# Kernel tuning notes

Measured on AMD Instinct MI355X. Metric: run time of the kernel, lower is better.

## Reference

```python
import jax, jax.numpy as jnp
import numpy as np
import math

H = 16          # num heads
D = 64          # size_per_head
HID = H * D     # 1024
ROT = 32        # rotary_hsize <= D//2


def setup_inputs() -> dict:
    key = jax.random.key(0)
    ks = jax.random.split(key, 10)
    B, S = 2, 2048
    x = jax.random.normal(ks[0], (B, S, HID), dtype=jnp.float32)
    sinusoids = jax.random.normal(ks[1], (B, 2, S, ROT), dtype=jnp.float32)
    attention_bias = jnp.zeros((B, 1, S, S), dtype=jnp.float32)
    scale = 1.0 / math.sqrt(HID)
    Wq = jax.random.normal(ks[2], (HID, HID), dtype=jnp.float32) * scale
    bq = jnp.zeros((HID,), dtype=jnp.float32)
    Wk = jax.random.normal(ks[3], (HID, HID), dtype=jnp.float32) * scale
    bk = jnp.zeros((HID,), dtype=jnp.float32)
    Wv = jax.random.normal(ks[4], (HID, HID), dtype=jnp.float32) * scale
    bv = jnp.zeros((HID,), dtype=jnp.float32)
    Wo = jax.random.normal(ks[5], (HID, HID), dtype=jnp.float32) * scale
    return {"x": x, "sinusoids": sinusoids, "attention_bias": attention_bias,
            "Wq": Wq, "bq": bq, "Wk": Wk, "bk": bk, "Wv": Wv, "bv": bv, "Wo": Wo}


def _apply_rotary(qk, sin, cos):
    # qk: [B,S,H,D]; sin/cos: [B,S,1,ROT]
    r = qk[..., :ROT]
    # stack([-even, odd], -1).reshape -> interleaved (-x0, x1, -x2, x3, ...)
    rt = jnp.stack([-r[..., ::2], r[..., 1::2]], axis=-1).reshape(r.shape)
    return jnp.concatenate([r * cos + rt * sin, qk[..., ROT:]], axis=-1)


def reference(x, sinusoids, attention_bias, Wq, bq, Wk, bk, Wv, bv, Wo):
    B, S, _ = x.shape
    q = (x @ Wq + bq).reshape(B, S, H, D)
    k = (x @ Wk + bk).reshape(B, S, H, D)
    v = (x @ Wv + bv).reshape(B, S, H, D)
    sin = sinusoids[..., 0, :, None, :]  # [B,S,1,ROT]
    cos = sinusoids[..., 1, :, None, :]
    q = _apply_rotary(q, sin, cos)
    k = _apply_rotary(k, sin, cos)
    q = q / math.sqrt(D)
    scores = jnp.einsum('bqhd,bkhd->bhqk', q, k) + attention_bias
    probs = jax.nn.softmax(scores, axis=-1)
    out = jnp.einsum('bhqk,bkhd->bqhd', probs, v).reshape(B, S, HID)
    return out @ Wo
```

## Files before the change

kernel.cpp:

```cpp
#include <hip/hip_runtime.h>
#include <hip/hip_bf16.h>

#define H_   16
#define D_   64
#define HID  1024
#define S_   2048
#define B_   2
#define M_   (B_*S_)
#define ROT  32
#define LOG2E 1.44269504088896341f
#define QSCALE (0.125f * LOG2E)

typedef __bf16 bf16x8 __attribute__((ext_vector_type(8)));
typedef float  f32x4  __attribute__((ext_vector_type(4)));

#define XB_OFF   0u
#define WQT_OFF  (8u<<20)
#define WKT_OFF  (10u<<20)
#define WVT_OFF  (12u<<20)
#define WOT_OFF  (14u<<20)
#define F_OFF    (16u<<20)
#define QH_OFF   ((16u<<20) + (1u<<19))
#define KH_OFF   (QH_OFF + (8u<<20))
#define VT_OFF   (KH_OFF + (8u<<20))
#define AB_OFF   (VT_OFF + (8u<<20))

__device__ __forceinline__ float fexp2(float x) {
#if __has_builtin(__builtin_amdgcn_exp2f)
  return __builtin_amdgcn_exp2f(x);
#else
  return __expf(x * 0.69314718055994531f);
#endif
}

__device__ __forceinline__ unsigned pk2(float a, float b) {
  union { unsigned u; __bf16 h[2]; } w;
  w.h[0] = (__bf16)a; w.h[1] = (__bf16)b;
  return w.u;
}

__global__ __launch_bounds__(256) void convx_kernel(const float* __restrict__ x,
                                                    __hip_bfloat16* __restrict__ xb,
                                                    int* __restrict__ flag) {
  if (blockIdx.x == 0 && threadIdx.x == 0) *flag = 0;
  int i = (blockIdx.x * 256 + threadIdx.x) * 4;
  float4 v = *(const float4*)(x + i);
  union { __hip_bfloat16 h[4]; uint2 u; } o;
  o.h[0] = __float2bfloat16(v.x);
  o.h[1] = __float2bfloat16(v.y);
  o.h[2] = __float2bfloat16(v.z);
  o.h[3] = __float2bfloat16(v.w);
  *(uint2*)(xb + i) = o.u;
}

__global__ __launch_bounds__(256) void biaschk_kernel(const float* __restrict__ ab,
                                                      int* __restrict__ flag) {
  size_t i = ((size_t)blockIdx.x * 256 + threadIdx.x) * 16;
  const uint4* p = (const uint4*)(ab + i);
  unsigned acc = 0;
  #pragma unroll
  for (int j = 0; j < 4; j++) {
    uint4 u = p[j];
    acc |= u.x | u.y | u.z | u.w;
  }
  if (acc) *flag = 1;
}

__global__ __launch_bounds__(256) void rotf_kernel(const float* __restrict__ sinu,
                                                   float* __restrict__ F) {
  int i = blockIdx.x * 256 + threadIdx.x;
  int d  = i & (ROT-1);
  int bs = i >> 5;
  int s  = bs & (S_-1);
  int b  = bs >> 11;
  float sn = sinu[(((size_t)b*2 + 0)*S_ + s)*ROT + d];
  float cs = sinu[(((size_t)b*2 + 1)*S_ + s)*ROT + d];
  F[i] = cs + ((d & 1) ? sn : -sn);
}

__global__ __launch_bounds__(256) void wtrans_kernel(const float* __restrict__ W0, const float* __restrict__ W1,
                                                     const float* __restrict__ W2, const float* __restrict__ W3,
                                                     __hip_bfloat16* __restrict__ T0, __hip_bfloat16* __restrict__ T1,
                                                     __hip_bfloat16* __restrict__ T2, __hip_bfloat16* __restrict__ T3) {
  __shared__ float tile[32][33];
  const float* W = (blockIdx.z==0) ? W0 : (blockIdx.z==1) ? W1 : (blockIdx.z==2) ? W2 : W3;
  __hip_bfloat16* T = (blockIdx.z==0) ? T0 : (blockIdx.z==1) ? T1 : (blockIdx.z==2) ? T2 : T3;
  int bx = blockIdx.x * 32;
  int by = blockIdx.y * 32;
  int tx = threadIdx.x, ty = threadIdx.y;
  #pragma unroll
  for (int i = 0; i < 4; i++)
    tile[ty + i*8][tx] = W[(size_t)(by + ty + i*8)*HID + bx + tx];
  __syncthreads();
  #pragma unroll
  for (int i = 0; i < 4; i++)
    T[(size_t)(bx + ty + i*8)*HID + by + tx] = __float2bfloat16(tile[tx][ty + i*8]);
}

__global__ __launch_bounds__(256) void qkv_kernel(const __hip_bfloat16* __restrict__ A,
                                                  const __hip_bfloat16* __restrict__ Bt,
                                                  const float* __restrict__ bq,
                                                  const float* __restrict__ bk,
                                                  const float* __restrict__ bv,
                                                  const float* __restrict__ F,
                                                  __hip_bfloat16* __restrict__ Qh,
                                                  __hip_bfloat16* __restrict__ Kh,
                                                  __hip_bfloat16* __restrict__ Vt) {
  __shared__ __align__(16) __bf16 Asm[2][128*32];
  __shared__ __align__(16) __bf16 Bsm[2][64*32];
  int tid  = threadIdx.x;
  int lane = tid & 63;
  int wv   = tid >> 6;
  int lr   = lane & 15;
  int qd   = lane >> 4;
  int row0 = blockIdx.y * 128;
  int col0 = blockIdx.x * 64;
  int proj = col0 >> 10;
  int nb   = col0 & 1023;
  const float* bias = (proj == 0) ? bq : ((proj == 1) ? bk : bv);

  int cg = ((tid & 3) ^ ((tid >> 2) & 3)) * 8;
  const __bf16* Ag = (const __bf16*)A  + (size_t)(row0 + (tid >> 2)) * HID + cg;
  const __bf16* Bg = (const __bf16*)Bt + (size_t)(col0 + (tid >> 2)) * HID + cg;

  f32x4 acc[2][4] = {};

  auto stage = [&](int buf, int k0) {
    __builtin_amdgcn_global_load_lds(Ag + k0,                  &Asm[buf][wv*512],        16, 0, 0);
    __builtin_amdgcn_global_load_lds(Ag + (size_t)64*HID + k0, &Asm[buf][2048 + wv*512], 16, 0, 0);
    __builtin_amdgcn_global_load_lds(Bg + k0,                  &Bsm[buf][wv*512],        16, 0, 0);
  };

  stage(0, 0);
  int buf = 0;
  for (int k0 = 0; k0 < HID; k0 += 32, buf ^= 1) {
    __syncthreads();
    if (k0 + 32 < HID) stage(buf ^ 1, k0 + 32);
    const __bf16* As = &Asm[buf][0];
    const __bf16* Bs = &Bsm[buf][0];
    bf16x8 a[2], b[4];
    #pragma unroll
    for (int i = 0; i < 2; i++) {
      int row = wv*32 + i*16 + lr;
      a[i] = *(const bf16x8*)(As + row*32 + ((qd ^ (row & 3)) * 8));
    }
    #pragma unroll
    for (int t = 0; t < 4; t++) {
      int row = t*16 + lr;
      b[t] = *(const bf16x8*)(Bs + row*32 + ((qd ^ (row & 3)) * 8));
    }
    #pragma unroll
    for (int i = 0; i < 2; i++)
      #pragma unroll
      for (int t = 0; t < 4; t++)
        acc[i][t] = __builtin_amdgcn_mfma_f32_16x16x32_bf16(a[i], b[t], acc[i][t], 0, 0, 0);
  }

  #pragma unroll
  for (int i = 0; i < 2; i++) {
    #pragma unroll
    for (int t = 0; t < 4; t++) {
      int nl = nb + t*16 + lr;
      int h  = nl >> 6, d = nl & 63;
      if (proj == 2) {
        int m0 = row0 + wv*32 + i*16 + qd*4;
        int b2 = m0 >> 11, s0 = m0 & (S_-1);
        union { uint2 u; __bf16 hh[4]; } w;
        #pragma unroll
        for (int r = 0; r < 4; r++)
          w.hh[r] = (__bf16)(acc[i][t][r] + bias[nl]);
        *(uint2*)((__bf16*)Vt + ((size_t)(b2*H_ + h)*D_ + d)*S_ + s0) = w.u;
      } else {
        __hip_bfloat16* dst = (proj == 0) ? Qh : Kh;
        #pragma unroll
        for (int r = 0; r < 4; r++) {
          int m = row0 + wv*32 + i*16 + qd*4 + r;
          int b2 = m >> 11, s = m & (S_-1);
          float v = acc[i][t][r] + bias[nl];
          if (d < ROT) v *= F[(size_t)(b2*S_ + s)*ROT + d];
          if (proj == 0) v *= QSCALE;
          dst[((size_t)(b2*H_ + h)*S_ + s)*D_ + d] = __float2bfloat16(v);
        }
      }
    }
  }
}

__global__ __launch_bounds__(256) void gemm_o(const __hip_bfloat16* __restrict__ A,
                                              const __hip_bfloat16* __restrict__ Bt,
                                              float* __restrict__ out) {
  __shared__ __align__(16) __bf16 Asm[2][128*32];
  __shared__ __align__(16) __bf16 Bsm[2][64*32];
  int tid  = threadIdx.x;
  int lane = tid & 63;
  int wv   = tid >> 6;
  int lr   = lane & 15;
  int qd   = lane >> 4;
  int row0 = blockIdx.y * 128;
  int col0 = blockIdx.x * 64;
  int cg = ((tid & 3) ^ ((tid >> 2) & 3)) * 8;
  const __bf16* Ag = (const __bf16*)A  + (size_t)(row0 + (tid >> 2)) * HID + cg;
  const __bf16* Bg = (const __bf16*)Bt + (size_t)(col0 + (tid >> 2)) * HID + cg;

  f32x4 acc[2][4] = {};
  auto stage = [&](int buf, int k0) {
    __builtin_amdgcn_global_load_lds(Ag + k0,                  &Asm[buf][wv*512],        16, 0, 0);
    __builtin_amdgcn_global_load_lds(Ag + (size_t)64*HID + k0, &Asm[buf][2048 + wv*512], 16, 0, 0);
    __builtin_amdgcn_global_load_lds(Bg + k0,                  &Bsm[buf][wv*512],        16, 0, 0);
  };
  stage(0, 0);
  int buf = 0;
  for (int k0 = 0; k0 < HID; k0 += 32, buf ^= 1) {
    __syncthreads();
    if (k0 + 32 < HID) stage(buf ^ 1, k0 + 32);
    const __bf16* As = &Asm[buf][0];
    const __bf16* Bs = &Bsm[buf][0];
    bf16x8 a[2], b[4];
    #pragma unroll
    for (int i = 0; i < 2; i++) {
      int row = wv*32 + i*16 + lr;
      a[i] = *(const bf16x8*)(As + row*32 + ((qd ^ (row & 3)) * 8));
    }
    #pragma unroll
    for (int t = 0; t < 4; t++) {
      int row = t*16 + lr;
      b[t] = *(const bf16x8*)(Bs + row*32 + ((qd ^ (row & 3)) * 8));
    }
    #pragma unroll
    for (int i = 0; i < 2; i++)
      #pragma unroll
      for (int t = 0; t < 4; t++)
        acc[i][t] = __builtin_amdgcn_mfma_f32_16x16x32_bf16(a[i], b[t], acc[i][t], 0, 0, 0);
  }
  #pragma unroll
  for (int i = 0; i < 2; i++)
    #pragma unroll
    for (int t = 0; t < 4; t++)
      #pragma unroll
      for (int r = 0; r < 4; r++) {
        int m = row0 + wv*32 + i*16 + qd*4 + r;
        int n = col0 + t*16 + lr;
        out[(size_t)m*HID + n] = acc[i][t][r];
      }
}

#define PSTRIDE 72
__global__ __launch_bounds__(256) void flash_kernel(const __hip_bfloat16* __restrict__ Qh,
                                                    const __hip_bfloat16* __restrict__ Kh,
                                                    const __hip_bfloat16* __restrict__ Vt,
                                                    const float* __restrict__ abias,
                                                    const int* __restrict__ flag,
                                                    __hip_bfloat16* __restrict__ Ab) {
  __shared__ __align__(16) __bf16 Ksm[2][64*64];
  __shared__ __align__(16) __bf16 Vsm[2][64*64];
  __shared__ __align__(16) __bf16 Pb[4][32*PSTRIDE];
  int tid  = threadIdx.x;
  int lane = tid & 63;
  int wv   = tid >> 6;
  int lr   = lane & 15;
  int qd   = lane >> 4;
  int bh = blockIdx.y;
  int b  = bh >> 4;
  int h  = bh & 15;
  int q0 = blockIdx.x * 128 + wv * 32;

  const __bf16* Kbase = (const __bf16*)Kh + (size_t)bh*S_*D_;
  const __bf16* Vbase = (const __bf16*)Vt + (size_t)bh*D_*S_;

  const __bf16* Qp = (const __bf16*)Qh + ((size_t)bh*S_ + q0 + lr)*D_ + qd*8;
  bf16x8 qa00 = *(const bf16x8*)(Qp);
  bf16x8 qa01 = *(const bf16x8*)(Qp + 32);
  bf16x8 qa10 = *(const bf16x8*)(Qp + 16*D_);
  bf16x8 qa11 = *(const bf16x8*)(Qp + 16*D_ + 32);

  int hasbias = *flag;
  const float* bp0 = abias + (size_t)b*S_*S_ + (size_t)(q0 + lr)*S_;
  const float* bp1 = bp0 + (size_t)16*S_;

  int rowb = tid >> 3;
  int cg8  = ((tid & 7) ^ (rowb & 7)) * 8;

  auto stageKV = [&](int bf, int kt2) {
    __builtin_amdgcn_global_load_lds(Kbase + (size_t)(kt2 + rowb)*D_ + cg8,      &Ksm[bf][wv*512],        16, 0, 0);
    __builtin_amdgcn_global_load_lds(Kbase + (size_t)(kt2 + 32 + rowb)*D_ + cg8, &Ksm[bf][2048 + wv*512], 16, 0, 0);
    __builtin_amdgcn_global_load_lds(Vbase + (size_t)rowb*S_ + kt2 + cg8,        &Vsm[bf][wv*512],        16, 0, 0);
    __builtin_amdgcn_global_load_lds(Vbase + (size_t)(32 + rowb)*S_ + kt2 + cg8, &Vsm[bf][2048 + wv*512], 16, 0, 0);
  };

  f32x4 oacc0[4] = {}, oacc1[4] = {};
  float lsum0 = 0.f, lsum1 = 0.f;
  __bf16* P = &Pb[wv][0];
  int sw = lr & 7;

  stageKV(0, 0);
  int buf = 0;
  for (int kt = 0; kt < S_; kt += 64, buf ^= 1) {
    __syncthreads();
    if (kt + 64 < S_) stageKV(buf ^ 1, kt + 64);

    bf16x8 kf0[4], kf1[4];
    #pragma unroll
    for (int c = 0; c < 4; c++) {
      const __bf16* Kr = &Ksm[buf][(c*16 + lr)*64];
      kf0[c] = *(const bf16x8*)(Kr + ((qd       ^ sw) * 8));
      kf1[c] = *(const bf16x8*)(Kr + (((4 + qd) ^ sw) * 8));
    }
    f32x4 s0[4], s1[4];
    #pragma unroll
    for (int c = 0; c < 4; c++) {
      f32x4 z = {};
      z     = __builtin_amdgcn_mfma_f32_16x16x32_bf16(kf0[c], qa00, z, 0, 0, 0);
      s0[c] = __builtin_amdgcn_mfma_f32_16x16x32_bf16(kf1[c], qa01, z, 0, 0, 0);
      f32x4 z2 = {};
      z2    = __builtin_amdgcn_mfma_f32_16x16x32_bf16(kf0[c], qa10, z2, 0, 0, 0);
      s1[c] = __builtin_amdgcn_mfma_f32_16x16x32_bf16(kf1[c], qa11, z2, 0, 0, 0);
    }
    bf16x8 vf0[4], vf1[4];
    #pragma unroll
    for (int t = 0; t < 4; t++) {
      const __bf16* Vr = &Vsm[buf][(t*16 + lr)*64];
      vf0[t] = *(const bf16x8*)(Vr + ((qd       ^ sw) * 8));
      vf1[t] = *(const bf16x8*)(Vr + (((4 + qd) ^ sw) * 8));
    }
    if (hasbias) {
      #pragma unroll
      for (int c = 0; c < 4; c++) {
        float4 b0 = *(const float4*)(bp0 + kt + c*16 + qd*4);
        float4 b1 = *(const float4*)(bp1 + kt + c*16 + qd*4);
        s0[c][0] += b0.x*LOG2E; s0[c][1] += b0.y*LOG2E; s0[c][2] += b0.z*LOG2E; s0[c][3] += b0.w*LOG2E;
        s1[c][0] += b1.x*LOG2E; s1[c][1] += b1.y*LOG2E; s1[c][2] += b1.z*LOG2E; s1[c][3] += b1.w*LOG2E;
      }
    }
    #pragma unroll
    for (int c = 0; c < 4; c++) {
      float p0 = fexp2(s0[c][0]), p1 = fexp2(s0[c][1]), p2 = fexp2(s0[c][2]), p3 = fexp2(s0[c][3]);
      lsum0 += (p0 + p1) + (p2 + p3);
      *(unsigned*)(P + lr*PSTRIDE + c*16 + qd*4)     = pk2(p0, p1);
      *(unsigned*)(P + lr*PSTRIDE + c*16 + qd*4 + 2) = pk2(p2, p3);
      float r0 = fexp2(s1[c][0]), r1 = fexp2(s1[c][1]), r2 = fexp2(s1[c][2]), r3 = fexp2(s1[c][3]);
      lsum1 += (r0 + r1) + (r2 + r3);
      *(unsigned*)(P + (16+lr)*PSTRIDE + c*16 + qd*4)     = pk2(r0, r1);
      *(unsigned*)(P + (16+lr)*PSTRIDE + c*16 + qd*4 + 2) = pk2(r2, r3);
    }
    asm volatile("s_waitcnt lgkmcnt(0)" ::: "memory");
    bf16x8 pb00 = *(const bf16x8*)(P + lr*PSTRIDE + qd*8);
    bf16x8 pb01 = *(const bf16x8*)(P + lr*PSTRIDE + 32 + qd*8);
    bf16x8 pb10 = *(const bf16x8*)(P + (16+lr)*PSTRIDE + qd*8);
    bf16x8 pb11 = *(const bf16x8*)(P + (16+lr)*PSTRIDE + 32 + qd*8);
    #pragma unroll
    for (int t = 0; t < 4; t++) {
      oacc0[t] = __builtin_amdgcn_mfma_f32_16x16x32_bf16(vf0[t], pb00, oacc0[t], 0, 0, 0);
      oacc0[t] = __builtin_amdgcn_mfma_f32_16x16x32_bf16(vf1[t], pb01, oacc0[t], 0, 0, 0);
      oacc1[t] = __builtin_amdgcn_mfma_f32_16x16x32_bf16(vf0[t], pb10, oacc1[t], 0, 0, 0);
      oacc1[t] = __builtin_amdgcn_mfma_f32_16x16x32_bf16(vf1[t], pb11, oacc1[t], 0, 0, 0);
    }
  }

  lsum0 += __shfl_xor(lsum0, 16); lsum0 += __shfl_xor(lsum0, 32);
  lsum1 += __shfl_xor(lsum1, 16); lsum1 += __shfl_xor(lsum1, 32);
  float inv0 = 1.0f / lsum0;
  float inv1 = 1.0f / lsum1;
  size_t ro0 = ((size_t)(b*S_ + q0 + lr))*HID + h*D_;
  size_t ro1 = ((size_t)(b*S_ + q0 + 16 + lr))*HID + h*D_;
  #pragma unroll
  for (int t = 0; t < 4; t++) {
    union { uint2 u; __bf16 hh[4]; } w0, w1;
    #pragma unroll
    for (int r = 0; r < 4; r++) {
      w0.hh[r] = (__bf16)(oacc0[t][r]*inv0);
      w1.hh[r] = (__bf16)(oacc1[t][r]*inv1);
    }
    *(uint2*)((__bf16*)Ab + ro0 + t*16 + qd*4) = w0.u;
    *(uint2*)((__bf16*)Ab + ro1 + t*16 + qd*4) = w1.u;
  }
}

extern "C" void kernel_launch(void* const* d_in, const int* in_sizes, int n_in,
                              void* d_out, int out_size, void* d_ws, size_t ws_size,
                              hipStream_t stream) {
  (void)in_sizes; (void)n_in; (void)out_size; (void)ws_size;
  const float* x     = (const float*)d_in[0];
  const float* sinu  = (const float*)d_in[1];
  const float* abias = (const float*)d_in[2];
  const float* Wq    = (const float*)d_in[3];
  const float* bq    = (const float*)d_in[4];
  const float* Wk    = (const float*)d_in[5];
  const float* bk    = (const float*)d_in[6];
  const float* Wv    = (const float*)d_in[7];
  const float* bv    = (const float*)d_in[8];
  const float* Wo    = (const float*)d_in[9];

  char* ws = (char*)d_ws;
  __hip_bfloat16* Xb  = (__hip_bfloat16*)(ws + XB_OFF);
  __hip_bfloat16* Wqt = (__hip_bfloat16*)(ws + WQT_OFF);
  __hip_bfloat16* Wkt = (__hip_bfloat16*)(ws + WKT_OFF);
  __hip_bfloat16* Wvt = (__hip_bfloat16*)(ws + WVT_OFF);
  __hip_bfloat16* Wot = (__hip_bfloat16*)(ws + WOT_OFF);
  float*          F   = (float*)(ws + F_OFF);
  __hip_bfloat16* Qh  = (__hip_bfloat16*)(ws + QH_OFF);
  __hip_bfloat16* Kh  = (__hip_bfloat16*)(ws + KH_OFF);
  __hip_bfloat16* Vt  = (__hip_bfloat16*)(ws + VT_OFF);
  __hip_bfloat16* Ab  = (__hip_bfloat16*)(ws + AB_OFF);
  int* flag = (int*)d_out;

  convx_kernel<<<(M_*HID)/(256*4), 256, 0, stream>>>(x, Xb, flag);
  rotf_kernel<<<(B_*S_*ROT)/256, 256, 0, stream>>>(sinu, F);
  wtrans_kernel<<<dim3(HID/32, HID/32, 4), dim3(32, 8), 0, stream>>>(
      Wq, Wk, Wv, Wo, Wqt, Wkt, Wvt, Wot);
  biaschk_kernel<<<(B_*S_*S_)/(256*16), 256, 0, stream>>>(abias, flag);

  qkv_kernel<<<dim3(3*HID/64, M_/128), 256, 0, stream>>>(
      Xb, Wqt, bq, bk, bv, F, Qh, Kh, Vt);

  flash_kernel<<<dim3(S_/128, B_*H_), 256, 0, stream>>>(Qh, Kh, Vt, abias, flag, Ab);

  gemm_o<<<dim3(HID/64, M_/128), 256, 0, stream>>>(Ab, Wot, (float*)d_out);
}
```

Baseline: 249.0 us.

## Enlarge GEMM tiles to 128x128 and remap flash blocks for XCD locality

The QKV and output-projection GEMMs are merged into one templated kernel that uses a 128x128 block tile, with each wave computing a 64x64 sub-tile (4x4 MFMA accumulators) instead of 32x64. The aim is more operand reuse per LDS load, at the cost of higher register pressure and fewer blocks. Flash attention is changed to a 1D grid remapped so that all query blocks of the same batch-head land on the same XCD, which should improve L2 reuse of K/V.

```diff
diff --git a/kernel.cpp b/kernel.cpp
--- a/kernel.cpp
+++ b/kernel.cpp
@@ -97,38 +97,40 @@
     T[(size_t)(bx + ty + i*8)*HID + by + tx] = __float2bfloat16(tile[tx][ty + i*8]);
 }
 
-__global__ __launch_bounds__(256) void qkv_kernel(const __hip_bfloat16* __restrict__ A,
-                                                  const __hip_bfloat16* __restrict__ Bt,
-                                                  const float* __restrict__ bq,
-                                                  const float* __restrict__ bk,
-                                                  const float* __restrict__ bv,
-                                                  const float* __restrict__ F,
-                                                  __hip_bfloat16* __restrict__ Qh,
-                                                  __hip_bfloat16* __restrict__ Kh,
-                                                  __hip_bfloat16* __restrict__ Vt) {
+template<int MODE>
+__global__ __launch_bounds__(256) void gemm128(const __hip_bfloat16* __restrict__ A,
+                                               const __hip_bfloat16* __restrict__ Bt,
+                                               const float* __restrict__ bq,
+                                               const float* __restrict__ bk,
+                                               const float* __restrict__ bv,
+                                               const float* __restrict__ F,
+                                               __hip_bfloat16* __restrict__ Qh,
+                                               __hip_bfloat16* __restrict__ Kh,
+                                               __hip_bfloat16* __restrict__ Vt,
+                                               float* __restrict__ outf) {
   __shared__ __align__(16) __bf16 Asm[2][128*32];
-  __shared__ __align__(16) __bf16 Bsm[2][64*32];
+  __shared__ __align__(16) __bf16 Bsm[2][128*32];
   int tid  = threadIdx.x;
   int lane = tid & 63;
   int wv   = tid >> 6;
   int lr   = lane & 15;
   int qd   = lane >> 4;
   int row0 = blockIdx.y * 128;
-  int col0 = blockIdx.x * 64;
-  int proj = col0 >> 10;
-  int nb   = col0 & 1023;
-  const float* bias = (proj == 0) ? bq : ((proj == 1) ? bk : bv);
+  int col0 = blockIdx.x * 128;
+  int wrow = (wv >> 1) * 64;
+  int wcol = (wv & 1) * 64;
 
   int cg = ((tid & 3) ^ ((tid >> 2) & 3)) * 8;
   const __bf16* Ag = (const __bf16*)A  + (size_t)(row0 + (tid >> 2)) * HID + cg;
   const __bf16* Bg = (const __bf16*)Bt + (size_t)(col0 + (tid >> 2)) * HID + cg;
 
-  f32x4 acc[2][4] = {};
+  f32x4 acc[4][4] = {};
 
   auto stage = [&](int buf, int k0) {
     __builtin_amdgcn_global_load_lds(Ag + k0,                  &Asm[buf][wv*512],        16, 0, 0);
     __builtin_amdgcn_global_load_lds(Ag + (size_t)64*HID + k0, &Asm[buf][2048 + wv*512], 16, 0, 0);
     __builtin_amdgcn_global_load_lds(Bg + k0,                  &Bsm[buf][wv*512],        16, 0, 0);
+    __builtin_amdgcn_global_load_lds(Bg + (size_t)64*HID + k0, &Bsm[buf][2048 + wv*512], 16, 0, 0);
   };
 
   stage(0, 0);
@@ -138,32 +140,49 @@
     if (k0 + 32 < HID) stage(buf ^ 1, k0 + 32);
     const __bf16* As = &Asm[buf][0];
     const __bf16* Bs = &Bsm[buf][0];
-    bf16x8 a[2], b[4];
-    #pragma unroll
-    for (int i = 0; i < 2; i++) {
-      int row = wv*32 + i*16 + lr;
+    bf16x8 a[4], b[4];
+    #pragma unroll
+    for (int i = 0; i < 4; i++) {
+      int row = wrow + i*16 + lr;
       a[i] = *(const bf16x8*)(As + row*32 + ((qd ^ (row & 3)) * 8));
     }
     #pragma unroll
     for (int t = 0; t < 4; t++) {
-      int row = t*16 + lr;
+      int row = wcol + t*16 + lr;
       b[t] = *(const bf16x8*)(Bs + row*32 + ((qd ^ (row & 3)) * 8));
     }
     #pragma unroll
-    for (int i = 0; i < 2; i++)
+    for (int i = 0; i < 4; i++)
       #pragma unroll
       for (int t = 0; t < 4; t++)
         acc[i][t] = __builtin_amdgcn_mfma_f32_16x16x32_bf16(a[i], b[t], acc[i][t], 0, 0, 0);
   }
 
-  #pragma unroll
-  for (int i = 0; i < 2; i++) {
+  if (MODE == 1) {
+    #pragma unroll
+    for (int i = 0; i < 4; i++)
+      #pragma unroll
+      for (int t = 0; t < 4; t++)
+        #pragma unroll
+        for (int r = 0; r < 4; r++) {
+          int m = row0 + wrow + i*16 + qd*4 + r;
+          int n = col0 + wcol + t*16 + lr;
+          outf[(size_t)m*HID + n] = acc[i][t][r];
+        }
+    return;
+  }
+
+  int proj = col0 >> 10;
+  int nb   = (col0 & 1023) + wcol;
+  const float* bias = (proj == 0) ? bq : ((proj == 1) ? bk : bv);
+  #pragma unroll
+  for (int i = 0; i < 4; i++) {
     #pragma unroll
     for (int t = 0; t < 4; t++) {
       int nl = nb + t*16 + lr;
       int h  = nl >> 6, d = nl & 63;
       if (proj == 2) {
-        int m0 = row0 + wv*32 + i*16 + qd*4;
+        int m0 = row0 + wrow + i*16 + qd*4;
         int b2 = m0 >> 11, s0 = m0 & (S_-1);
         union { uint2 u; __bf16 hh[4]; } w;
         #pragma unroll
@@ -174,7 +193,7 @@
         __hip_bfloat16* dst = (proj == 0) ? Qh : Kh;
         #pragma unroll
         for (int r = 0; r < 4; r++) {
-          int m = row0 + wv*32 + i*16 + qd*4 + r;
+          int m = row0 + wrow + i*16 + qd*4 + r;
           int b2 = m >> 11, s = m & (S_-1);
           float v = acc[i][t][r] + bias[nl];
           if (d < ROT) v *= F[(size_t)(b2*S_ + s)*ROT + d];
@@ -184,64 +203,6 @@
       }
     }
   }
-}
-
-__global__ __launch_bounds__(256) void gemm_o(const __hip_bfloat16* __restrict__ A,
-                                              const __hip_bfloat16* __restrict__ Bt,
-                                              float* __restrict__ out) {
-  __shared__ __align__(16) __bf16 Asm[2][128*32];
-  __shared__ __align__(16) __bf16 Bsm[2][64*32];
-  int tid  = threadIdx.x;
-  int lane = tid & 63;
-  int wv   = tid >> 6;
-  int lr   = lane & 15;
-  int qd   = lane >> 4;
-  int row0 = blockIdx.y * 128;
-  int col0 = blockIdx.x * 64;
-  int cg = ((tid & 3) ^ ((tid >> 2) & 3)) * 8;
-  const __bf16* Ag = (const __bf16*)A  + (size_t)(row0 + (tid >> 2)) * HID + cg;
-  const __bf16* Bg = (const __bf16*)Bt + (size_t)(col0 + (tid >> 2)) * HID + cg;
-
-  f32x4 acc[2][4] = {};
-  auto stage = [&](int buf, int k0) {
-    __builtin_amdgcn_global_load_lds(Ag + k0,                  &Asm[buf][wv*512],        16, 0, 0);
-    __builtin_amdgcn_global_load_lds(Ag + (size_t)64*HID + k0, &Asm[buf][2048 + wv*512], 16, 0, 0);
-    __builtin_amdgcn_global_load_lds(Bg + k0,                  &Bsm[buf][wv*512],        16, 0, 0);
-  };
-  stage(0, 0);
-  int buf = 0;
-  for (int k0 = 0; k0 < HID; k0 += 32, buf ^= 1) {
-    __syncthreads();
-    if (k0 + 32 < HID) stage(buf ^ 1, k0 + 32);
-    const __bf16* As = &Asm[buf][0];
-    const __bf16* Bs = &Bsm[buf][0];
-    bf16x8 a[2], b[4];
-    #pragma unroll
-    for (int i = 0; i < 2; i++) {
-      int row = wv*32 + i*16 + lr;
-      a[i] = *(const bf16x8*)(As + row*32 + ((qd ^ (row & 3)) * 8));
-    }
-    #pragma unroll
-    for (int t = 0; t < 4; t++) {
-      int row = t*16 + lr;
-      b[t] = *(const bf16x8*)(Bs + row*32 + ((qd ^ (row & 3)) * 8));
-    }
-    #pragma unroll
-    for (int i = 0; i < 2; i++)
-      #pragma unroll
-      for (int t = 0; t < 4; t++)
-        acc[i][t] = __builtin_amdgcn_mfma_f32_16x16x32_bf16(a[i], b[t], acc[i][t], 0, 0, 0);
-  }
-  #pragma unroll
-  for (int i = 0; i < 2; i++)
-    #pragma unroll
-    for (int t = 0; t < 4; t++)
-      #pragma unroll
-      for (int r = 0; r < 4; r++) {
-        int m = row0 + wv*32 + i*16 + qd*4 + r;
-        int n = col0 + t*16 + lr;
-        out[(size_t)m*HID + n] = acc[i][t][r];
-      }
 }
 
 #define PSTRIDE 72
@@ -259,10 +220,14 @@
   int wv   = tid >> 6;
   int lr   = lane & 15;
   int qd   = lane >> 4;
-  int bh = blockIdx.y;
+  int idx  = blockIdx.x;
+  int xcd  = idx & 7;
+  int slot = idx >> 3;
+  int bh   = xcd * 4 + (slot >> 4);
+  int qblk = slot & 15;
   int b  = bh >> 4;
   int h  = bh & 15;
-  int q0 = blockIdx.x * 128 + wv * 32;
+  int q0 = qblk * 128 + wv * 32;
 
   const __bf16* Kbase = (const __bf16*)Kh + (size_t)bh*S_*D_;
   const __bf16* Vbase = (const __bf16*)Vt + (size_t)bh*D_*S_;
@@ -409,10 +374,11 @@
       Wq, Wk, Wv, Wo, Wqt, Wkt, Wvt, Wot);
   biaschk_kernel<<<(B_*S_*S_)/(256*16), 256, 0, stream>>>(abias, flag);
 
-  qkv_kernel<<<dim3(3*HID/64, M_/128), 256, 0, stream>>>(
-      Xb, Wqt, bq, bk, bv, F, Qh, Kh, Vt);
-
-  flash_kernel<<<dim3(S_/128, B_*H_), 256, 0, stream>>>(Qh, Kh, Vt, abias, flag, Ab);
-
-  gemm_o<<<dim3(HID/64, M_/128), 256, 0, stream>>>(Ab, Wot, (float*)d_out);
-}
+  gemm128<0><<<dim3(3*HID/128, M_/128), 256, 0, stream>>>(
+      Xb, Wqt, bq, bk, bv, F, Qh, Kh, Vt, nullptr);
+
+  flash_kernel<<<dim3((S_/128) * B_ * H_), 256, 0, stream>>>(Qh, Kh, Vt, abias, flag, Ab);
+
+  gemm128<1><<<dim3(HID/128, M_/128), 256, 0, stream>>>(
+      Ab, Wot, nullptr, nullptr, nullptr, nullptr, nullptr, nullptr, nullptr, (float*)d_out);
+}
```

Measured after the change: 232.8 us. -6.5%, faster.
